# Kernel tuning notes

Hardware: AMD Instinct MI355X
Metric: run time of the kernel (lower is better)

The kernel has to match this reference:

```python
import jax, jax.numpy as jnp
import numpy as np

B, N_ENT, E, T, DEPTH, N_TREES = 512, 2000, 512, 512, 6, 2
N_LEAVES = 2 ** DEPTH  # 64


def setup_inputs() -> dict:
    key = jax.random.key(0)
    ks = jax.random.split(key, 20)
    s = lambda fan_in: 1.0 / np.sqrt(fan_in)
    inp = {
        "leaf_idx": jax.random.randint(ks[0], (B, N_TREES, N_LEAVES), 0, N_ENT),
        "ent_emb": jax.random.normal(ks[1], (N_ENT, E), jnp.float32),
        "th_emb": jax.random.normal(ks[2], (T,), jnp.float32),
        # two2one: Linear(2E,4E) ReLU Linear(4E,E) ReLU
        "w1": jax.random.normal(ks[3], (2 * E, 4 * E), jnp.float32) * s(2 * E),
        "b1": jnp.zeros((4 * E,), jnp.float32),
        "w2": jax.random.normal(ks[4], (4 * E, E), jnp.float32) * s(4 * E),
        "b2": jnp.zeros((E,), jnp.float32),
        # one2one: Linear(E,4E) ReLU Linear(4E,E) Tanh
        "o1": jax.random.normal(ks[5], (E, 4 * E), jnp.float32) * s(E),
        "ob1": jnp.zeros((4 * E,), jnp.float32),
        "o2": jax.random.normal(ks[6], (4 * E, E), jnp.float32) * s(4 * E),
        "ob2": jnp.zeros((E,), jnp.float32),
        # theorem head: (T + 2E) -> E -> E/2 -> E/4 -> 1
        "h1": jax.random.normal(ks[7], (T + N_TREES * E, E), jnp.float32) * s(T + N_TREES * E),
        "hb1": jnp.zeros((E,), jnp.float32),
        "h2": jax.random.normal(ks[8], (E, E // 2), jnp.float32) * s(E),
        "hb2": jnp.zeros((E // 2,), jnp.float32),
        "h3": jax.random.normal(ks[9], (E // 2, E // 4), jnp.float32) * s(E // 2),
        "hb3": jnp.zeros((E // 4,), jnp.float32),
        "h4": jax.random.normal(ks[10], (E // 4, 1), jnp.float32) * s(E // 4),
        "hb4": jnp.zeros((1,), jnp.float32),
    }
    return inp


def _two2one(x, w1, b1, w2, b2):
    # x: [..., n_pairs, 2E] -> [..., n_pairs, E]  (ReLU, ReLU)
    h = jax.nn.relu(x @ w1 + b1)
    return jax.nn.relu(h @ w2 + b2)


def _one2one(x, o1, ob1, o2, ob2):
    # ReLU then Tanh, as in one2one_layers
    h = jax.nn.relu(x @ o1 + ob1)
    return jnp.tanh(h @ o2 + ob2)


def reference(leaf_idx, ent_emb, th_emb, w1, b1, w2, b2, o1, ob1, o2, ob2,
              h1, hb1, h2, hb2, h3, hb3, h4, hb4):
    # Leaf embedding lookups: [B, N_TREES, N_LEAVES, E]
    x = ent_emb[leaf_idx]
    # Level-by-level binary tree reduction with the two2one MLP
    n = N_LEAVES
    while n > 1:
        x = x.reshape(B, N_TREES, n // 2, 2 * E)
        x = _two2one(x, w1, b1, w2, b2)
        n //= 2
    root = x.reshape(B, N_TREES, E)
    # Unary numerical function applied at each entity root (Tanh output)
    root = _one2one(root, o1, ob1, o2, ob2)
    # Theorem head: concat theorem embedding with the entity encodings
    feat = jnp.concatenate(
        [jnp.broadcast_to(th_emb, (B, T)), root.reshape(B, N_TREES * E)], axis=-1)
    z = jax.nn.relu(feat @ h1 + hb1)
    z = jax.nn.relu(z @ h2 + hb2)
    z = jax.nn.relu(z @ h3 + hb3)
    return jax.nn.sigmoid(z @ h4 + hb4)  # [B, 1]
```

## Files before the change

### kernel.cpp

```cpp
#include <hip/hip_runtime.h>
#include <cstddef>
#include <cstdint>


typedef _Float16 f16;
typedef _Float16 f16x8 __attribute__((ext_vector_type(8)));
typedef float f32x4 __attribute__((ext_vector_type(4)));

__device__ __forceinline__ void gll16(const void* g, void* l) {
  __builtin_amdgcn_global_load_lds(
      (const __attribute__((address_space(1))) void*)g,
      (__attribute__((address_space(3))) void*)l, 16, 0, 0);
}

#define BAR __builtin_amdgcn_s_barrier()
#define VM6 asm volatile("s_waitcnt vmcnt(6)" ::: "memory")
#define VM0 asm volatile("s_waitcnt vmcnt(0)" ::: "memory")

template <int GATHER>
__global__ __launch_bounds__(512) void gemm8(
    const f16* __restrict__ A, const f16* __restrict__ Bt,
    const float* __restrict__ bias, f16* __restrict__ C, int N, int K,
    const int* __restrict__ lidx, const f16* __restrict__ entf) {
  __shared__ __align__(16) f16 As[2][2][128][64];
  __shared__ __align__(16) f16 Bs[2][2][128][64];
  const int tid = threadIdx.x;
  const int m0 = blockIdx.y * 256;
  const int n0 = blockIdx.x * 256;

  const int srow = tid >> 3;
  const int sk = ((tid & 7) ^ (srow & 7)) << 3;
  const int wvb = (tid >> 6) * 1024;
  const f16* Asrc = GATHER ? (const f16*)nullptr
                           : (A + (size_t)(m0 + srow) * K + sk);
  const f16* Bsrc = Bt + (size_t)(n0 + srow) * K + sk;

  int eA0[2][2], eA1[2][2];
  if (GATHER) {
#pragma unroll
    for (int hh = 0; hh < 2; ++hh)
#pragma unroll
      for (int oo = 0; oo < 2; ++oo) {
        const int grow = m0 + hh * 128 + oo * 64 + srow;
        eA0[hh][oo] = lidx[2 * grow];
        eA1[hh][oo] = lidx[2 * grow + 1];
      }
  }

#define STAGE_A(BUF, HALF, KB)                                          \
  {                                                                     \
    char* d_ = (char*)&As[BUF][HALF][0][0] + wvb;                       \
    if (!GATHER) {                                                      \
      const f16* s_ = Asrc + (size_t)((HALF)*128) * K + (KB);           \
      gll16(s_, d_);                                                    \
      gll16(s_ + (size_t)64 * K, d_ + 8192);                            \
    } else {                                                            \
      const int hs_ = (KB) >> 9;                                        \
      const int kk_ = ((KB)&511) + sk;                                  \
      const int e0_ = hs_ ? eA1[HALF][0] : eA0[HALF][0];                \
      const int e1_ = hs_ ? eA1[HALF][1] : eA0[HALF][1];                \
      gll16(entf + ((size_t)e0_ << 9) + kk_, d_);                       \
      gll16(entf + ((size_t)e1_ << 9) + kk_, d_ + 8192);                \
    }                                                                   \
  }
#define STAGE_B(BUF, HALF, KB)                                          \
  {                                                                     \
    char* d_ = (char*)&Bs[BUF][HALF][0][0] + wvb;                       \
    const f16* s_ = Bsrc + (size_t)((HALF)*128) * K + (KB);             \
    gll16(s_, d_);                                                      \
    gll16(s_ + (size_t)64 * K, d_ + 8192);                              \
  }

  const int l = tid & 63, wid = tid >> 6;
  const int wm = wid >> 2, wn = wid & 3;
  const int q = l & 15, kg = l >> 4;
  const char* Ard = (const char*)&As[0][wm][0][0] + q * 128;
  const char* Brd = (const char*)&Bs[0][wn >> 1][0][0] + ((wn & 1) * 64 + q) * 128;
  const int csw = (kg << 4) ^ ((q & 7) << 4);

  f16x8 a[8][2], b[4][2];
  f32x4 acc[8][4] = {};

#define RD_AB(BUF)                                                          \
  {                                                                         \
    _Pragma("unroll") for (int i_ = 0; i_ < 8; ++i_) {                      \
      a[i_][0] = *(const f16x8*)(Ard + (BUF)*32768 + i_ * 2048 + csw);      \
      a[i_][1] = *(const f16x8*)(Ard + (BUF)*32768 + i_ * 2048 + (csw ^ 64)); \
    }                                                                       \
    _Pragma("unroll") for (int j_ = 0; j_ < 4; ++j_) {                      \
      b[j_][0] = *(const f16x8*)(Brd + (BUF)*32768 + j_ * 2048 + csw);      \
      b[j_][1] = *(const f16x8*)(Brd + (BUF)*32768 + j_ * 2048 + (csw ^ 64)); \
    }                                                                       \
  }
#define MM(MLO, KS)                                                         \
  __builtin_amdgcn_s_setprio(1);                                            \
  {                                                                         \
    _Pragma("unroll") for (int i_ = 0; i_ < 4; ++i_) {                      \
      _Pragma("unroll") for (int j_ = 0; j_ < 4; ++j_) {                    \
        acc[(MLO)*4 + i_][j_] = __builtin_amdgcn_mfma_f32_16x16x32_f16(     \
            a[(MLO)*4 + i_][KS], b[j_][KS], acc[(MLO)*4 + i_][j_], 0, 0, 0); \
      }                                                                     \
    }                                                                       \
  }                                                                         \
  __builtin_amdgcn_s_setprio(0);

  STAGE_A(0, 0, 0); STAGE_A(0, 1, 0); STAGE_B(0, 0, 0); STAGE_B(0, 1, 0);
  STAGE_A(1, 0, 64); STAGE_A(1, 1, 64); STAGE_B(1, 0, 64);
  VM6; BAR;

  const int niter = K >> 7;
  int kb = 0;
  for (int it = 0; it < niter - 1; ++it, kb += 128) {
    const int t1 = kb + 64, t2 = kb + 128, t3 = kb + 192;
    RD_AB(0); STAGE_B(1, 1, t1);      BAR; MM(0, 0); BAR;
    STAGE_A(0, 0, t2);                BAR; MM(1, 0); BAR;
    STAGE_A(0, 1, t2);                BAR; MM(0, 1); BAR;
    STAGE_B(0, 0, t2);           VM6; BAR; MM(1, 1); BAR;
    RD_AB(1); STAGE_B(0, 1, t2);      BAR; MM(0, 0); BAR;
    STAGE_A(1, 0, t3);                BAR; MM(1, 0); BAR;
    STAGE_A(1, 1, t3);                BAR; MM(0, 1); BAR;
    STAGE_B(1, 0, t3);           VM6; BAR; MM(1, 1); BAR;
  }
  {
    const int t1 = kb + 64;
    RD_AB(0); STAGE_B(1, 1, t1);      BAR; MM(0, 0); BAR;
                                      BAR; MM(1, 0); BAR;
                                      BAR; MM(0, 1); BAR;
                                 VM0; BAR; MM(1, 1); BAR;
    RD_AB(1);                         BAR; MM(0, 0); BAR;
                                      BAR; MM(1, 0); BAR;
                                      BAR; MM(0, 1); BAR;
                                      BAR; MM(1, 1); BAR;
  }
#undef STAGE_A
#undef STAGE_B
#undef RD_AB
#undef MM

#pragma unroll
  for (int j = 0; j < 4; ++j) {
    const int col = n0 + wn * 64 + j * 16 + q;
    const float bsv = bias[col];
#pragma unroll
    for (int i = 0; i < 8; ++i) {
      f32x4 v = acc[i][j];
#pragma unroll
      for (int vi = 0; vi < 4; ++vi) {
        const int row = m0 + wm * 128 + i * 16 + kg * 4 + vi;
        float c = fmaxf(v[vi] + bsv, 0.0f);
        C[(size_t)row * N + col] = (f16)c;
      }
    }
  }
}

template <int ACT, int OUTF32>
__global__ __launch_bounds__(256) void gemm128(
    const f16* __restrict__ A, const f16* __restrict__ Bt,
    const float* __restrict__ bias, void* __restrict__ Cout, int N, int K) {
  __shared__ __align__(16) f16 As[128 * 64];
  __shared__ __align__(16) f16 Bs[128 * 64];
  const int tid = threadIdx.x;
  const int m0 = blockIdx.y * 128;
  const int n0 = blockIdx.x * 128;
  const int srow = tid >> 3;
  const int sk = ((tid & 7) ^ ((tid >> 3) & 7)) << 3;
  const f16* Ag = A + (size_t)(m0 + srow) * K + sk;
  const f16* Bg = Bt + (size_t)(n0 + srow) * K + sk;
  char* Al = (char*)As + (tid >> 6) * 1024;
  char* Bl = (char*)Bs + (tid >> 6) * 1024;
  const int l = tid & 63;
  const int wm = tid >> 7;
  const int wn = (tid >> 6) & 1;
  const int q = l & 15;
  const int kg = l >> 4;
  const char* Ar = (const char*)As + (wm * 64 + q) * 128;
  const char* Br = (const char*)Bs + (wn * 64 + q) * 128;
  const int c0 = ((kg << 4) ^ ((q & 7) << 4));
  f32x4 acc[4][4] = {};
  for (int k0 = 0; k0 < K; k0 += 64) {
#pragma unroll
    for (int r = 0; r < 4; ++r) {
      gll16(Ag + (size_t)(r * 32) * K + k0, Al + r * 4096);
      gll16(Bg + (size_t)(r * 32) * K + k0, Bl + r * 4096);
    }
    __syncthreads();
#pragma unroll
    for (int ks = 0; ks < 2; ++ks) {
      const int cb = c0 ^ (ks << 6);
      f16x8 a[4], b[4];
#pragma unroll
      for (int i = 0; i < 4; ++i) a[i] = *(const f16x8*)(Ar + i * 2048 + cb);
#pragma unroll
      for (int j = 0; j < 4; ++j) b[j] = *(const f16x8*)(Br + j * 2048 + cb);
#pragma unroll
      for (int i = 0; i < 4; ++i)
#pragma unroll
        for (int j = 0; j < 4; ++j)
          acc[i][j] = __builtin_amdgcn_mfma_f32_16x16x32_f16(a[i], b[j],
                                                             acc[i][j], 0, 0, 0);
    }
    __syncthreads();
  }
#pragma unroll
  for (int j = 0; j < 4; ++j) {
    const int col = n0 + wn * 64 + j * 16 + q;
    const float bsv = bias[col];
#pragma unroll
    for (int i = 0; i < 4; ++i) {
      f32x4 v = acc[i][j];
#pragma unroll
      for (int vi = 0; vi < 4; ++vi) {
        const int row = m0 + wm * 64 + i * 16 + kg * 4 + vi;
        float c = v[vi] + bsv;
        if (ACT == 1) c = fmaxf(c, 0.0f);
        if (ACT == 2) c = tanhf(c);
        if (OUTF32)
          ((float*)Cout)[(size_t)row * N + col] = c;
        else
          ((f16*)Cout)[(size_t)row * N + col] = (f16)c;
      }
    }
  }
}

__global__ void transpose_cvt(const float* __restrict__ src,
                              f16* __restrict__ dst, int K, int N) {
  __shared__ f16 tile[32][33];
  const int k0 = blockIdx.x * 32, n0 = blockIdx.y * 32;
  const int tx = threadIdx.x & 31, ty = threadIdx.x >> 5;
  for (int r = ty; r < 32; r += 8)
    tile[r][tx] = (f16)src[(size_t)(k0 + r) * N + n0 + tx];
  __syncthreads();
  for (int r = ty; r < 32; r += 8)
    dst[(size_t)(n0 + r) * K + k0 + tx] = tile[tx][r];
}

__global__ void cvt_f16(const float* __restrict__ src, f16* __restrict__ dst) {
  const int g = blockIdx.x * 256 + threadIdx.x;
  const float4* s = (const float4*)(src + (size_t)g * 8);
  float4 v0 = s[0], v1 = s[1];
  f16x8 o;
  o[0] = (f16)v0.x; o[1] = (f16)v0.y; o[2] = (f16)v0.z; o[3] = (f16)v0.w;
  o[4] = (f16)v1.x; o[5] = (f16)v1.y; o[6] = (f16)v1.z; o[7] = (f16)v1.w;
  *(f16x8*)(dst + (size_t)g * 8) = o;
}

__global__ void build_feat_h(const float* __restrict__ th,
                             const f16* __restrict__ root,
                             f16* __restrict__ feat) {
  int idx = blockIdx.x * 256 + threadIdx.x;
  int b = idx / 1536;
  int c = idx - b * 1536;
  feat[idx] = (c < 512) ? (f16)th[c] : root[(size_t)b * 1024 + (c - 512)];
}

__global__ void head_final(const float* __restrict__ z3,
                           const float* __restrict__ h4,
                           const float* __restrict__ hb4,
                           float* __restrict__ out) {
  int row = blockIdx.x;
  int t = threadIdx.x;
  float v = z3[(size_t)row * 128 + t] * h4[t] +
            z3[(size_t)row * 128 + 64 + t] * h4[64 + t];
#pragma unroll
  for (int off = 32; off; off >>= 1) v += __shfl_down(v, off);
  if (t == 0) out[row] = 1.0f / (1.0f + expf(-(v + hb4[0])));
}

extern "C" void kernel_launch(void* const* d_in, const int* in_sizes, int n_in,
                              void* d_out, int out_size, void* d_ws,
                              size_t ws_size, hipStream_t stream) {
  const int* leaf_idx = (const int*)d_in[0];
  const float* ent_emb = (const float*)d_in[1];
  const float* th_emb = (const float*)d_in[2];
  const float* w1 = (const float*)d_in[3];
  const float* b1 = (const float*)d_in[4];
  const float* w2 = (const float*)d_in[5];
  const float* b2 = (const float*)d_in[6];
  const float* o1 = (const float*)d_in[7];
  const float* ob1 = (const float*)d_in[8];
  const float* o2 = (const float*)d_in[9];
  const float* ob2 = (const float*)d_in[10];
  const float* h1 = (const float*)d_in[11];
  const float* hb1 = (const float*)d_in[12];
  const float* h2 = (const float*)d_in[13];
  const float* hb2 = (const float*)d_in[14];
  const float* h3 = (const float*)d_in[15];
  const float* hb3 = (const float*)d_in[16];
  const float* h4 = (const float*)d_in[17];
  const float* hb4 = (const float*)d_in[18];
  float* out = (float*)d_out;

  char* p = (char*)d_ws;
  f16* w1t = (f16*)p;  p += (size_t)2048 * 1024 * 2;
  f16* w2t = (f16*)p;  p += (size_t)512 * 2048 * 2;
  f16* o1t = (f16*)p;  p += (size_t)2048 * 512 * 2;
  f16* o2t = (f16*)p;  p += (size_t)512 * 2048 * 2;
  f16* h1t = (f16*)p;  p += (size_t)512 * 1536 * 2;
  f16* h2t = (f16*)p;  p += (size_t)256 * 512 * 2;
  f16* h3t = (f16*)p;  p += (size_t)128 * 256 * 2;
  f16* entf = (f16*)p; p += (size_t)2000 * 512 * 2;
  f16* Hf   = (f16*)p; p += (size_t)32768 * 2048 * 2;
  f16* bufA = (f16*)p; p += (size_t)32768 * 512 * 2;
  f16* featf = (f16*)p; p += (size_t)512 * 1536 * 2;
  f16* z1h  = (f16*)p; p += (size_t)512 * 512 * 2;
  f16* z2h  = (f16*)p; p += (size_t)512 * 256 * 2;
  float* z3 = (float*)p; p += (size_t)512 * 128 * 4;
  f16* bufB = Hf + (size_t)32 * 1024 * 1024;

  transpose_cvt<<<dim3(1024 / 32, 2048 / 32), 256, 0, stream>>>(w1, w1t, 1024, 2048);
  transpose_cvt<<<dim3(2048 / 32, 512 / 32), 256, 0, stream>>>(w2, w2t, 2048, 512);
  transpose_cvt<<<dim3(512 / 32, 2048 / 32), 256, 0, stream>>>(o1, o1t, 512, 2048);
  transpose_cvt<<<dim3(2048 / 32, 512 / 32), 256, 0, stream>>>(o2, o2t, 2048, 512);
  transpose_cvt<<<dim3(1536 / 32, 512 / 32), 256, 0, stream>>>(h1, h1t, 1536, 512);
  transpose_cvt<<<dim3(512 / 32, 256 / 32), 256, 0, stream>>>(h2, h2t, 512, 256);
  transpose_cvt<<<dim3(256 / 32, 128 / 32), 256, 0, stream>>>(h3, h3t, 256, 128);
  cvt_f16<<<(2000 * 512) / 2048, 256, 0, stream>>>(ent_emb, entf);

  gemm8<1><<<dim3(8, 128), 512, 0, stream>>>(nullptr, w1t, b1, Hf, 2048, 1024,
                                             leaf_idx, entf);
  gemm8<0><<<dim3(2, 128), 512, 0, stream>>>(Hf, w2t, b2, bufA, 512, 2048,
                                             nullptr, nullptr);
  gemm8<0><<<dim3(8, 64), 512, 0, stream>>>(bufA, w1t, b1, Hf, 2048, 1024,
                                            nullptr, nullptr);
  gemm128<1, 0><<<dim3(4, 128), 256, 0, stream>>>(Hf, w2t, b2, bufB, 512, 2048);
  gemm8<0><<<dim3(8, 32), 512, 0, stream>>>(bufB, w1t, b1, Hf, 2048, 1024,
                                            nullptr, nullptr);
  gemm128<1, 0><<<dim3(4, 64), 256, 0, stream>>>(Hf, w2t, b2, bufA, 512, 2048);
  gemm128<1, 0><<<dim3(16, 32), 256, 0, stream>>>(bufA, w1t, b1, Hf, 2048, 1024);
  gemm128<1, 0><<<dim3(4, 32), 256, 0, stream>>>(Hf, w2t, b2, bufB, 512, 2048);
  gemm128<1, 0><<<dim3(16, 16), 256, 0, stream>>>(bufB, w1t, b1, Hf, 2048, 1024);
  gemm128<1, 0><<<dim3(4, 16), 256, 0, stream>>>(Hf, w2t, b2, bufA, 512, 2048);
  gemm128<1, 0><<<dim3(16, 8), 256, 0, stream>>>(bufA, w1t, b1, Hf, 2048, 1024);
  gemm128<1, 0><<<dim3(4, 8), 256, 0, stream>>>(Hf, w2t, b2, bufB, 512, 2048);

  gemm128<1, 0><<<dim3(16, 8), 256, 0, stream>>>(bufB, o1t, ob1, Hf, 2048, 512);
  gemm128<2, 0><<<dim3(4, 8), 256, 0, stream>>>(Hf, o2t, ob2, bufA, 512, 2048);

  build_feat_h<<<(512 * 1536) / 256, 256, 0, stream>>>(th_emb, bufA, featf);
  gemm128<1, 0><<<dim3(4, 4), 256, 0, stream>>>(featf, h1t, hb1, z1h, 512, 1536);
  gemm128<1, 0><<<dim3(2, 4), 256, 0, stream>>>(z1h, h2t, hb2, z2h, 256, 512);
  gemm128<1, 1><<<dim3(1, 4), 256, 0, stream>>>(z2h, h3t, hb3, z3, 128, 256);
  head_final<<<512, 64, 0, stream>>>(z3, h4, hb4, out);
}
```

Baseline: 989.9 us.

## Restructure big GEMM into triple-buffered K=32 pipeline with two blocks per CU

Replaces the 256x256 GEMM kernel's double-buffered K=64 LDS staging with a three-stage ring of K=32 slices and a new XOR swizzle. It also sets launch_bounds(512,2). Shared memory per block drops from 128KB to 96KB, which could let two 512-thread blocks share a CU and overlap one block's loads with the other's MFMA work. In exchange each tile does twice as many barriers per unit of K and fewer MFMAs between syncs, and the register cap may cause spills.

```diff
diff --git a/kernel.cpp b/kernel.cpp
--- a/kernel.cpp
+++ b/kernel.cpp
@@ -14,127 +14,108 @@
 }
 
 #define BAR __builtin_amdgcn_s_barrier()
-#define VM6 asm volatile("s_waitcnt vmcnt(6)" ::: "memory")
+#define VM4 asm volatile("s_waitcnt vmcnt(4)" ::: "memory")
 #define VM0 asm volatile("s_waitcnt vmcnt(0)" ::: "memory")
 
 template <int GATHER>
-__global__ __launch_bounds__(512) void gemm8(
+__global__ __launch_bounds__(512, 2) void gemm4(
     const f16* __restrict__ A, const f16* __restrict__ Bt,
     const float* __restrict__ bias, f16* __restrict__ C, int N, int K,
     const int* __restrict__ lidx, const f16* __restrict__ entf) {
-  __shared__ __align__(16) f16 As[2][2][128][64];
-  __shared__ __align__(16) f16 Bs[2][2][128][64];
+  __shared__ __align__(16) f16 As[3][256][32];
+  __shared__ __align__(16) f16 Bs[3][256][32];
   const int tid = threadIdx.x;
   const int m0 = blockIdx.y * 256;
   const int n0 = blockIdx.x * 256;
 
-  const int srow = tid >> 3;
-  const int sk = ((tid & 7) ^ (srow & 7)) << 3;
+  const int srow = tid >> 2;
+  const int fs = (((tid & 3) ^ ((srow & 3) ^ ((srow >> 2) & 3)))) << 3;
+  const f16* Asrc = GATHER ? (const f16*)nullptr
+                           : (A + (size_t)(m0 + srow) * K + fs);
+  const f16* Bsrc = Bt + (size_t)(n0 + srow) * K + fs;
   const int wvb = (tid >> 6) * 1024;
-  const f16* Asrc = GATHER ? (const f16*)nullptr
-                           : (A + (size_t)(m0 + srow) * K + sk);
-  const f16* Bsrc = Bt + (size_t)(n0 + srow) * K + sk;
-
-  int eA0[2][2], eA1[2][2];
+
+  int eh0[2], eh1[2];
   if (GATHER) {
 #pragma unroll
-    for (int hh = 0; hh < 2; ++hh)
-#pragma unroll
-      for (int oo = 0; oo < 2; ++oo) {
-        const int grow = m0 + hh * 128 + oo * 64 + srow;
-        eA0[hh][oo] = lidx[2 * grow];
-        eA1[hh][oo] = lidx[2 * grow + 1];
-      }
-  }
-
-#define STAGE_A(BUF, HALF, KB)                                          \
-  {                                                                     \
-    char* d_ = (char*)&As[BUF][HALF][0][0] + wvb;                       \
-    if (!GATHER) {                                                      \
-      const f16* s_ = Asrc + (size_t)((HALF)*128) * K + (KB);           \
-      gll16(s_, d_);                                                    \
-      gll16(s_ + (size_t)64 * K, d_ + 8192);                            \
-    } else {                                                            \
-      const int hs_ = (KB) >> 9;                                        \
-      const int kk_ = ((KB)&511) + sk;                                  \
-      const int e0_ = hs_ ? eA1[HALF][0] : eA0[HALF][0];                \
-      const int e1_ = hs_ ? eA1[HALF][1] : eA0[HALF][1];                \
-      gll16(entf + ((size_t)e0_ << 9) + kk_, d_);                       \
-      gll16(entf + ((size_t)e1_ << 9) + kk_, d_ + 8192);                \
-    }                                                                   \
-  }
-#define STAGE_B(BUF, HALF, KB)                                          \
-  {                                                                     \
-    char* d_ = (char*)&Bs[BUF][HALF][0][0] + wvb;                       \
-    const f16* s_ = Bsrc + (size_t)((HALF)*128) * K + (KB);             \
-    gll16(s_, d_);                                                      \
-    gll16(s_ + (size_t)64 * K, d_ + 8192);                              \
+    for (int h = 0; h < 2; ++h) {
+      const int grow = m0 + h * 128 + srow;
+      eh0[h] = lidx[2 * grow];
+      eh1[h] = lidx[2 * grow + 1];
+    }
+  }
+
+#define STAGE_A(S, H, KB)                                              \
+  {                                                                    \
+    char* d_ = (char*)As + (size_t)(S)*16384 + (H)*8192 + wvb;         \
+    if (!GATHER) {                                                     \
+      gll16(Asrc + (size_t)(H)*128 * K + (KB), d_);                    \
+    } else {                                                           \
+      const int e_ = ((KB) >> 9) ? eh1[H] : eh0[H];                    \
+      gll16(entf + ((size_t)e_ << 9) + (((KB)&511) + fs), d_);         \
+    }                                                                  \
+  }
+#define STAGE_B(S, H, KB)                                              \
+  {                                                                    \
+    char* d_ = (char*)Bs + (size_t)(S)*16384 + (H)*8192 + wvb;         \
+    gll16(Bsrc + (size_t)(H)*128 * K + (KB), d_);                      \
   }
 
   const int l = tid & 63, wid = tid >> 6;
   const int wm = wid >> 2, wn = wid & 3;
   const int q = l & 15, kg = l >> 4;
-  const char* Ard = (const char*)&As[0][wm][0][0] + q * 128;
-  const char* Brd = (const char*)&Bs[0][wn >> 1][0][0] + ((wn & 1) * 64 + q) * 128;
-  const int csw = (kg << 4) ^ ((q & 7) << 4);
-
-  f16x8 a[8][2], b[4][2];
+  const int fq = (q & 3) ^ ((q >> 2) & 3);
+  const int csw = (kg ^ fq) << 4;
+  const char* Ard = (const char*)As + (wm * 128 + q) * 64 + csw;
+  const char* Brd = (const char*)Bs + (wn * 64 + q) * 64 + csw;
+
+  f16x8 a[8], b[4];
   f32x4 acc[8][4] = {};
 
-#define RD_AB(BUF)                                                          \
-  {                                                                         \
-    _Pragma("unroll") for (int i_ = 0; i_ < 8; ++i_) {                      \
-      a[i_][0] = *(const f16x8*)(Ard + (BUF)*32768 + i_ * 2048 + csw);      \
-      a[i_][1] = *(const f16x8*)(Ard + (BUF)*32768 + i_ * 2048 + (csw ^ 64)); \
-    }                                                                       \
-    _Pragma("unroll") for (int j_ = 0; j_ < 4; ++j_) {                      \
-      b[j_][0] = *(const f16x8*)(Brd + (BUF)*32768 + j_ * 2048 + csw);      \
-      b[j_][1] = *(const f16x8*)(Brd + (BUF)*32768 + j_ * 2048 + (csw ^ 64)); \
-    }                                                                       \
-  }
-#define MM(MLO, KS)                                                         \
-  __builtin_amdgcn_s_setprio(1);                                            \
-  {                                                                         \
-    _Pragma("unroll") for (int i_ = 0; i_ < 4; ++i_) {                      \
-      _Pragma("unroll") for (int j_ = 0; j_ < 4; ++j_) {                    \
-        acc[(MLO)*4 + i_][j_] = __builtin_amdgcn_mfma_f32_16x16x32_f16(     \
-            a[(MLO)*4 + i_][KS], b[j_][KS], acc[(MLO)*4 + i_][j_], 0, 0, 0); \
-      }                                                                     \
-    }                                                                       \
-  }                                                                         \
+#define RD(S)                                                          \
+  {                                                                    \
+    _Pragma("unroll") for (int i_ = 0; i_ < 8; ++i_)                   \
+        a[i_] = *(const f16x8*)(Ard + (S)*16384 + i_ * 1024);          \
+    _Pragma("unroll") for (int j_ = 0; j_ < 4; ++j_)                   \
+        b[j_] = *(const f16x8*)(Brd + (S)*16384 + j_ * 1024);          \
+  }
+#define MM(MLO)                                                        \
+  __builtin_amdgcn_s_setprio(1);                                       \
+  {                                                                    \
+    _Pragma("unroll") for (int i_ = 0; i_ < 4; ++i_) {                 \
+      _Pragma("unroll") for (int j_ = 0; j_ < 4; ++j_) {               \
+        acc[(MLO)*4 + i_][j_] = __builtin_amdgcn_mfma_f32_16x16x32_f16( \
+            a[(MLO)*4 + i_], b[j_], acc[(MLO)*4 + i_][j_], 0, 0, 0);   \
+      }                                                                \
+    }                                                                  \
+  }                                                                    \
   __builtin_amdgcn_s_setprio(0);
 
   STAGE_A(0, 0, 0); STAGE_A(0, 1, 0); STAGE_B(0, 0, 0); STAGE_B(0, 1, 0);
-  STAGE_A(1, 0, 64); STAGE_A(1, 1, 64); STAGE_B(1, 0, 64);
-  VM6; BAR;
-
-  const int niter = K >> 7;
-  int kb = 0;
-  for (int it = 0; it < niter - 1; ++it, kb += 128) {
-    const int t1 = kb + 64, t2 = kb + 128, t3 = kb + 192;
-    RD_AB(0); STAGE_B(1, 1, t1);      BAR; MM(0, 0); BAR;
-    STAGE_A(0, 0, t2);                BAR; MM(1, 0); BAR;
-    STAGE_A(0, 1, t2);                BAR; MM(0, 1); BAR;
-    STAGE_B(0, 0, t2);           VM6; BAR; MM(1, 1); BAR;
-    RD_AB(1); STAGE_B(0, 1, t2);      BAR; MM(0, 0); BAR;
-    STAGE_A(1, 0, t3);                BAR; MM(1, 0); BAR;
-    STAGE_A(1, 1, t3);                BAR; MM(0, 1); BAR;
-    STAGE_B(1, 0, t3);           VM6; BAR; MM(1, 1); BAR;
-  }
-  {
-    const int t1 = kb + 64;
-    RD_AB(0); STAGE_B(1, 1, t1);      BAR; MM(0, 0); BAR;
-                                      BAR; MM(1, 0); BAR;
-                                      BAR; MM(0, 1); BAR;
-                                 VM0; BAR; MM(1, 1); BAR;
-    RD_AB(1);                         BAR; MM(0, 0); BAR;
-                                      BAR; MM(1, 0); BAR;
-                                      BAR; MM(0, 1); BAR;
-                                      BAR; MM(1, 1); BAR;
+  STAGE_A(1, 0, 32); STAGE_A(1, 1, 32); STAGE_B(1, 0, 32); STAGE_B(1, 1, 32);
+  VM4; BAR;
+
+  const int nt = K >> 5;
+  int s = 0;
+  for (int t = 0; t < nt; ++t) {
+    const int s2 = (s + 2 >= 3) ? (s - 1) : (s + 2);
+    const int kb2 = (t + 2) << 5;
+    const bool pf = (t + 2) < nt;
+    RD(s);
+    if (pf) { STAGE_A(s2, 0, kb2); STAGE_A(s2, 1, kb2); }
+    BAR; MM(0); BAR;
+    if (pf) {
+      STAGE_B(s2, 0, kb2); STAGE_B(s2, 1, kb2);
+      VM4;
+    } else {
+      VM0;
+    }
+    BAR; MM(1); BAR;
+    s = (s + 1 == 3) ? 0 : (s + 1);
   }
 #undef STAGE_A
 #undef STAGE_B
-#undef RD_AB
+#undef RD
 #undef MM
 
 #pragma unroll
@@ -147,8 +128,7 @@
 #pragma unroll
       for (int vi = 0; vi < 4; ++vi) {
         const int row = m0 + wm * 128 + i * 16 + kg * 4 + vi;
-        float c = fmaxf(v[vi] + bsv, 0.0f);
-        C[(size_t)row * N + col] = (f16)c;
+        C[(size_t)row * N + col] = (f16)fmaxf(v[vi] + bsv, 0.0f);
       }
     }
   }
@@ -318,14 +298,14 @@
   transpose_cvt<<<dim3(256 / 32, 128 / 32), 256, 0, stream>>>(h3, h3t, 256, 128);
   cvt_f16<<<(2000 * 512) / 2048, 256, 0, stream>>>(ent_emb, entf);
 
-  gemm8<1><<<dim3(8, 128), 512, 0, stream>>>(nullptr, w1t, b1, Hf, 2048, 1024,
+  gemm4<1><<<dim3(8, 128), 512, 0, stream>>>(nullptr, w1t, b1, Hf, 2048, 1024,
                                              leaf_idx, entf);
-  gemm8<0><<<dim3(2, 128), 512, 0, stream>>>(Hf, w2t, b2, bufA, 512, 2048,
+  gemm4<0><<<dim3(2, 128), 512, 0, stream>>>(Hf, w2t, b2, bufA, 512, 2048,
                                              nullptr, nullptr);
-  gemm8<0><<<dim3(8, 64), 512, 0, stream>>>(bufA, w1t, b1, Hf, 2048, 1024,
+  gemm4<0><<<dim3(8, 64), 512, 0, stream>>>(bufA, w1t, b1, Hf, 2048, 1024,
                                             nullptr, nullptr);
   gemm128<1, 0><<<dim3(4, 128), 256, 0, stream>>>(Hf, w2t, b2, bufB, 512, 2048);
-  gemm8<0><<<dim3(8, 32), 512, 0, stream>>>(bufB, w1t, b1, Hf, 2048, 1024,
+  gemm4<0><<<dim3(8, 32), 512, 0, stream>>>(bufB, w1t, b1, Hf, 2048, 1024,
                                             nullptr, nullptr);
   gemm128<1, 0><<<dim3(4, 64), 256, 0, stream>>>(Hf, w2t, b2, bufA, 512, 2048);
   gemm128<1, 0><<<dim3(16, 32), 256, 0, stream>>>(bufA, w1t, b1, Hf, 2048, 1024);
```

New measurement: 897.2 us. -9.4%, faster.

## Restructure 256x256 GEMM pipeline to load A fragments per quarter-step

Applied to the files above, without the earlier changes.

The 256x256 MFMA GEMM kernel now reads A fragments from LDS in small per-substep groups instead of all 8x2 at once, which cuts the register footprint. It also reorders the global-to-LDS staging so A tiles are prefetched in the loop rather than in the prologue, and merges the loop epilogue into the main loop using predicated prefetch. It adds launch_bounds(512,1) and changes the wait threshold to vmcnt(4). The aim is to lower register pressure and simplify the pipeline, at the cost of more frequent LDS reads and a different load/compute overlap pattern.

```diff
diff --git a/kernel.cpp b/kernel.cpp
--- a/kernel.cpp
+++ b/kernel.cpp
@@ -14,11 +14,11 @@
 }
 
 #define BAR __builtin_amdgcn_s_barrier()
-#define VM6 asm volatile("s_waitcnt vmcnt(6)" ::: "memory")
+#define VM4 asm volatile("s_waitcnt vmcnt(4)" ::: "memory")
 #define VM0 asm volatile("s_waitcnt vmcnt(0)" ::: "memory")
 
 template <int GATHER>
-__global__ __launch_bounds__(512) void gemm8(
+__global__ __launch_bounds__(512, 1) void gemm256(
     const f16* __restrict__ A, const f16* __restrict__ Bt,
     const float* __restrict__ bias, f16* __restrict__ C, int N, int K,
     const int* __restrict__ lidx, const f16* __restrict__ entf) {
@@ -30,24 +30,24 @@
 
   const int srow = tid >> 3;
   const int sk = ((tid & 7) ^ (srow & 7)) << 3;
-  const int wvb = (tid >> 6) * 1024;
   const f16* Asrc = GATHER ? (const f16*)nullptr
                            : (A + (size_t)(m0 + srow) * K + sk);
   const f16* Bsrc = Bt + (size_t)(n0 + srow) * K + sk;
-
-  int eA0[2][2], eA1[2][2];
+  const int wvb = (tid >> 6) * 1024;
+
+  int e0[2][2], e1[2][2];
   if (GATHER) {
 #pragma unroll
-    for (int hh = 0; hh < 2; ++hh)
-#pragma unroll
-      for (int oo = 0; oo < 2; ++oo) {
-        const int grow = m0 + hh * 128 + oo * 64 + srow;
-        eA0[hh][oo] = lidx[2 * grow];
-        eA1[hh][oo] = lidx[2 * grow + 1];
+    for (int h = 0; h < 2; ++h)
+#pragma unroll
+      for (int o = 0; o < 2; ++o) {
+        const int grow = m0 + h * 128 + o * 64 + srow;
+        e0[h][o] = lidx[2 * grow];
+        e1[h][o] = lidx[2 * grow + 1];
       }
   }
 
-#define STAGE_A(BUF, HALF, KB)                                          \
+#define SA(BUF, HALF, KB)                                               \
   {                                                                     \
     char* d_ = (char*)&As[BUF][HALF][0][0] + wvb;                       \
     if (!GATHER) {                                                      \
@@ -57,13 +57,13 @@
     } else {                                                            \
       const int hs_ = (KB) >> 9;                                        \
       const int kk_ = ((KB)&511) + sk;                                  \
-      const int e0_ = hs_ ? eA1[HALF][0] : eA0[HALF][0];                \
-      const int e1_ = hs_ ? eA1[HALF][1] : eA0[HALF][1];                \
-      gll16(entf + ((size_t)e0_ << 9) + kk_, d_);                       \
-      gll16(entf + ((size_t)e1_ << 9) + kk_, d_ + 8192);                \
+      const int ea_ = hs_ ? e1[HALF][0] : e0[HALF][0];                  \
+      const int eb_ = hs_ ? e1[HALF][1] : e0[HALF][1];                  \
+      gll16(entf + ((size_t)ea_ << 9) + kk_, d_);                       \
+      gll16(entf + ((size_t)eb_ << 9) + kk_, d_ + 8192);                \
     }                                                                   \
   }
-#define STAGE_B(BUF, HALF, KB)                                          \
+#define SB(BUF, HALF, KB)                                               \
   {                                                                     \
     char* d_ = (char*)&Bs[BUF][HALF][0][0] + wvb;                       \
     const f16* s_ = Bsrc + (size_t)((HALF)*128) * K + (KB);             \
@@ -74,67 +74,63 @@
   const int l = tid & 63, wid = tid >> 6;
   const int wm = wid >> 2, wn = wid & 3;
   const int q = l & 15, kg = l >> 4;
-  const char* Ard = (const char*)&As[0][wm][0][0] + q * 128;
-  const char* Brd = (const char*)&Bs[0][wn >> 1][0][0] + ((wn & 1) * 64 + q) * 128;
   const int csw = (kg << 4) ^ ((q & 7) << 4);
-
-  f16x8 a[8][2], b[4][2];
+  const char* Abase = (const char*)As + wm * 16384 + q * 128;
+  const char* Bbase =
+      (const char*)Bs + (wn >> 1) * 16384 + ((wn & 1) * 64 + q) * 128;
+
+  f16x8 a[4], b[4][2];
   f32x4 acc[8][4] = {};
 
-#define RD_AB(BUF)                                                          \
-  {                                                                         \
-    _Pragma("unroll") for (int i_ = 0; i_ < 8; ++i_) {                      \
-      a[i_][0] = *(const f16x8*)(Ard + (BUF)*32768 + i_ * 2048 + csw);      \
-      a[i_][1] = *(const f16x8*)(Ard + (BUF)*32768 + i_ * 2048 + (csw ^ 64)); \
-    }                                                                       \
-    _Pragma("unroll") for (int j_ = 0; j_ < 4; ++j_) {                      \
-      b[j_][0] = *(const f16x8*)(Brd + (BUF)*32768 + j_ * 2048 + csw);      \
-      b[j_][1] = *(const f16x8*)(Brd + (BUF)*32768 + j_ * 2048 + (csw ^ 64)); \
-    }                                                                       \
-  }
-#define MM(MLO, KS)                                                         \
-  __builtin_amdgcn_s_setprio(1);                                            \
-  {                                                                         \
-    _Pragma("unroll") for (int i_ = 0; i_ < 4; ++i_) {                      \
-      _Pragma("unroll") for (int j_ = 0; j_ < 4; ++j_) {                    \
-        acc[(MLO)*4 + i_][j_] = __builtin_amdgcn_mfma_f32_16x16x32_f16(     \
-            a[(MLO)*4 + i_][KS], b[j_][KS], acc[(MLO)*4 + i_][j_], 0, 0, 0); \
-      }                                                                     \
-    }                                                                       \
-  }                                                                         \
+#define RD_B(BUF)                                                       \
+  {                                                                     \
+    _Pragma("unroll") for (int j_ = 0; j_ < 4; ++j_) {                  \
+      b[j_][0] = *(const f16x8*)(Bbase + (BUF)*32768 + j_ * 2048 + csw);       \
+      b[j_][1] = *(const f16x8*)(Bbase + (BUF)*32768 + j_ * 2048 + (csw ^ 64)); \
+    }                                                                   \
+  }
+#define RD_A(BUF, HI, KS)                                               \
+  {                                                                     \
+    _Pragma("unroll") for (int i_ = 0; i_ < 4; ++i_)                    \
+        a[i_] = *(const f16x8*)(Abase + (BUF)*32768 +                   \
+                                ((HI)*4 + i_) * 2048 + (csw ^ ((KS) << 6))); \
+  }
+#define MM(HI, KS)                                                      \
+  __builtin_amdgcn_s_setprio(1);                                        \
+  {                                                                     \
+    _Pragma("unroll") for (int i_ = 0; i_ < 4; ++i_) {                  \
+      _Pragma("unroll") for (int j_ = 0; j_ < 4; ++j_) {                \
+        acc[(HI)*4 + i_][j_] = __builtin_amdgcn_mfma_f32_16x16x32_f16(  \
+            a[i_], b[j_][KS], acc[(HI)*4 + i_][j_], 0, 0, 0);           \
+      }                                                                 \
+    }                                                                   \
+  }                                                                     \
   __builtin_amdgcn_s_setprio(0);
 
-  STAGE_A(0, 0, 0); STAGE_A(0, 1, 0); STAGE_B(0, 0, 0); STAGE_B(0, 1, 0);
-  STAGE_A(1, 0, 64); STAGE_A(1, 1, 64); STAGE_B(1, 0, 64);
-  VM6; BAR;
+  SA(0, 0, 0); SA(0, 1, 0); SB(0, 0, 0); SB(0, 1, 0);
+  SB(1, 0, 64); SB(1, 1, 64);
+  VM4; BAR;
 
   const int niter = K >> 7;
-  int kb = 0;
-  for (int it = 0; it < niter - 1; ++it, kb += 128) {
-    const int t1 = kb + 64, t2 = kb + 128, t3 = kb + 192;
-    RD_AB(0); STAGE_B(1, 1, t1);      BAR; MM(0, 0); BAR;
-    STAGE_A(0, 0, t2);                BAR; MM(1, 0); BAR;
-    STAGE_A(0, 1, t2);                BAR; MM(0, 1); BAR;
-    STAGE_B(0, 0, t2);           VM6; BAR; MM(1, 1); BAR;
-    RD_AB(1); STAGE_B(0, 1, t2);      BAR; MM(0, 0); BAR;
-    STAGE_A(1, 0, t3);                BAR; MM(1, 0); BAR;
-    STAGE_A(1, 1, t3);                BAR; MM(0, 1); BAR;
-    STAGE_B(1, 0, t3);           VM6; BAR; MM(1, 1); BAR;
-  }
-  {
-    const int t1 = kb + 64;
-    RD_AB(0); STAGE_B(1, 1, t1);      BAR; MM(0, 0); BAR;
-                                      BAR; MM(1, 0); BAR;
-                                      BAR; MM(0, 1); BAR;
-                                 VM0; BAR; MM(1, 1); BAR;
-    RD_AB(1);                         BAR; MM(0, 0); BAR;
-                                      BAR; MM(1, 0); BAR;
-                                      BAR; MM(0, 1); BAR;
-                                      BAR; MM(1, 1); BAR;
-  }
-#undef STAGE_A
-#undef STAGE_B
-#undef RD_AB
+  for (int it = 0; it < niter; ++it) {
+    const int kt1 = (2 * it + 1) << 6;
+    const int kt2 = (2 * it + 2) << 6;
+    const int kt3 = (2 * it + 3) << 6;
+    const bool pf = (it + 1) < niter;
+    RD_B(0); RD_A(0, 0, 0); SA(1, 0, kt1);            BAR; MM(0, 0); BAR;
+    RD_A(0, 1, 0); SA(1, 1, kt1);                     BAR; MM(1, 0); BAR;
+    RD_A(0, 0, 1); if (pf) SB(0, 0, kt2);             BAR; MM(0, 1); BAR;
+    RD_A(0, 1, 1); if (pf) SB(0, 1, kt2);
+    if (pf) { VM4; } else { VM0; }                    BAR; MM(1, 1); BAR;
+    RD_B(1); RD_A(1, 0, 0); if (pf) SA(0, 0, kt2);    BAR; MM(0, 0); BAR;
+    RD_A(1, 1, 0); if (pf) SA(0, 1, kt2);             BAR; MM(1, 0); BAR;
+    RD_A(1, 0, 1); if (pf) SB(1, 0, kt3);             BAR; MM(0, 1); BAR;
+    RD_A(1, 1, 1); if (pf) { SB(1, 1, kt3); VM4; }    BAR; MM(1, 1); BAR;
+  }
+#undef SA
+#undef SB
+#undef RD_B
+#undef RD_A
 #undef MM
 
 #pragma unroll
@@ -147,8 +143,7 @@
 #pragma unroll
       for (int vi = 0; vi < 4; ++vi) {
         const int row = m0 + wm * 128 + i * 16 + kg * 4 + vi;
-        float c = fmaxf(v[vi] + bsv, 0.0f);
-        C[(size_t)row * N + col] = (f16)c;
+        C[(size_t)row * N + col] = (f16)fmaxf(v[vi] + bsv, 0.0f);
       }
     }
   }
@@ -318,15 +313,15 @@
   transpose_cvt<<<dim3(256 / 32, 128 / 32), 256, 0, stream>>>(h3, h3t, 256, 128);
   cvt_f16<<<(2000 * 512) / 2048, 256, 0, stream>>>(ent_emb, entf);
 
-  gemm8<1><<<dim3(8, 128), 512, 0, stream>>>(nullptr, w1t, b1, Hf, 2048, 1024,
-                                             leaf_idx, entf);
-  gemm8<0><<<dim3(2, 128), 512, 0, stream>>>(Hf, w2t, b2, bufA, 512, 2048,
-                                             nullptr, nullptr);
-  gemm8<0><<<dim3(8, 64), 512, 0, stream>>>(bufA, w1t, b1, Hf, 2048, 1024,
-                                            nullptr, nullptr);
+  gemm256<1><<<dim3(8, 128), 512, 0, stream>>>(nullptr, w1t, b1, Hf, 2048,
+                                               1024, leaf_idx, entf);
+  gemm256<0><<<dim3(2, 128), 512, 0, stream>>>(Hf, w2t, b2, bufA, 512, 2048,
+                                               nullptr, nullptr);
+  gemm256<0><<<dim3(8, 64), 512, 0, stream>>>(bufA, w1t, b1, Hf, 2048, 1024,
+                                              nullptr, nullptr);
   gemm128<1, 0><<<dim3(4, 128), 256, 0, stream>>>(Hf, w2t, b2, bufB, 512, 2048);
-  gemm8<0><<<dim3(8, 32), 512, 0, stream>>>(bufB, w1t, b1, Hf, 2048, 1024,
-                                            nullptr, nullptr);
+  gemm256<0><<<dim3(8, 32), 512, 0, stream>>>(bufB, w1t, b1, Hf, 2048, 1024,
+                                              nullptr, nullptr);
   gemm128<1, 0><<<dim3(4, 64), 256, 0, stream>>>(Hf, w2t, b2, bufA, 512, 2048);
   gemm128<1, 0><<<dim3(16, 32), 256, 0, stream>>>(bufA, w1t, b1, Hf, 2048, 1024);
   gemm128<1, 0><<<dim3(4, 32), 256, 0, stream>>>(Hf, w2t, b2, bufB, 512, 2048);
```

New measurement: 832.1 us. -15.9%, faster.
